# Kernel tuning notes

Measured on AMD Instinct MI355X. Metric: run time of the kernel, lower is better.

The kernel has to match this reference:

```python
import jax, jax.numpy as jnp
import numpy as np

EPS = 1e-8
CHUNK = 4096  # points per chunk, mirrors max_v_per_call-style tiling


def _winding_field(verts, faces, points):
    """Winding-number occupancy of `points` w.r.t. triangle mesh (verts, faces).
    verts: (V,3) f32, faces: (F,3) int, points: (P,3) f32 -> (P,) f32."""
    fv = verts[faces]                      # (F,3,3) face corner coords
    A = fv[:, 1] - fv[:, 0]
    B = fv[:, 2] - fv[:, 1]
    C = fv[:, 0] - fv[:, 2]

    def corner_angle(u, v):
        c = -jnp.sum(u * v, axis=1) / (EPS + jnp.linalg.norm(u, axis=1) * jnp.linalg.norm(v, axis=1))
        return jnp.arccos(jnp.clip(c, -1.0, 1.0))

    angles = jnp.stack([corner_angle(C, A), corner_angle(A, B), corner_angle(B, C)], axis=1)  # (F,3)
    s2 = jnp.sin(2.0 * angles)
    w = s2 / (jnp.sum(s2, axis=-1, keepdims=True) + EPS)
    w = (w[:, [2, 0, 1]] + w[:, [1, 2, 0]]) / 2.0     # dual area weights per corner

    fn = jnp.cross(A, B)                                # unnormalized face normals (F,3)
    areas = 0.5 * jnp.linalg.norm(fn, axis=1)           # face areas (F,)

    V = verts.shape[0]
    idx = faces.reshape(-1)                             # (3F,)
    # dual area per vertex: scatter-sum corner dual areas
    dual_v = jax.ops.segment_sum((w * areas[:, None]).reshape(-1), idx, num_segments=V)  # (V,)
    # area-weighted vertex normals: scatter-sum face normals to corners, then normalize
    vn = jax.ops.segment_sum(jnp.repeat(fn, 3, axis=0), idx, num_segments=V)             # (V,3)
    vn = vn / (jnp.linalg.norm(vn, axis=1, keepdims=True) + EPS)
    na = vn * dual_v[:, None]                           # areaic normals (V,3)

    def chunk_fn(p):                                    # p: (CHUNK,3)
        diff = verts[None, :, :] - p[:, None, :]        # (CHUNK,V,3)  == (p_vert - q_point)
        r = jnp.linalg.norm(diff, axis=-1, keepdims=True)
        E = diff / (r ** 3 + EPS)                       # 1/r^2 field direction
        return jnp.einsum('mvc,vc->m', E, na)           # (CHUNK,)

    P = points.shape[0]
    wf = jax.lax.map(chunk_fn, points.reshape(P // CHUNK, CHUNK, 3)).reshape(P)
    return wf / (4.0 * jnp.pi)


def setup_inputs() -> dict:
    key = jax.random.key(0)
    k1, k2, k3 = jax.random.split(key, 3)
    V, F, P = 8192, 16384, 32768
    verts = jax.random.uniform(k1, (V, 3), dtype=jnp.float32) * 2.0 - 1.0
    points = jax.random.uniform(k3, (P, 3), dtype=jnp.float32) * 2.0 - 1.0
    faces = jax.random.randint(k2, (F, 3), 0, V)
    return {"verts": verts, "points": points, "faces": faces}


def reference(verts, points, faces):
    return _winding_field(verts, faces, points)
```

## Files before the change

### kernel.cpp

```cpp
#include <hip/hip_runtime.h>
#include <math.h>

#define EPS32   1e-8f
#define INV4PI  0.07957747154594767f
#define TPB     256
#define VSLICE  128
#define PPT     4

__global__ void zero2_k(float* __restrict__ a, int na,
                        float* __restrict__ b, int nb) {
    int i = blockIdx.x * TPB + threadIdx.x;
    if (i < na) a[i] = 0.0f;
    else if (i < na + nb) b[i - na] = 0.0f;
}

__device__ __forceinline__ float n3_f32(float x, float y, float z) {
    return __fsqrt_rn(__fadd_rn(__fadd_rn(__fmul_rn(x, x), __fmul_rn(y, y)),
                                __fmul_rn(z, z)));
}

__global__ void face_k(const float* __restrict__ verts,
                       const int*   __restrict__ faces,
                       float*       __restrict__ acc, int F) {
    int f = blockIdx.x * TPB + threadIdx.x;
    if (f >= F) return;
    int i0 = faces[3*f+0], i1 = faces[3*f+1], i2 = faces[3*f+2];
    float p0x = verts[3*i0], p0y = verts[3*i0+1], p0z = verts[3*i0+2];
    float p1x = verts[3*i1], p1y = verts[3*i1+1], p1z = verts[3*i1+2];
    float p2x = verts[3*i2], p2y = verts[3*i2+1], p2z = verts[3*i2+2];

    float Ax = __fsub_rn(p1x, p0x), Ay = __fsub_rn(p1y, p0y), Az = __fsub_rn(p1z, p0z);
    float Bx = __fsub_rn(p2x, p1x), By = __fsub_rn(p2y, p1y), Bz = __fsub_rn(p2z, p1z);
    float Cx = __fsub_rn(p0x, p2x), Cy = __fsub_rn(p0y, p2y), Cz = __fsub_rn(p0z, p2z);

    float nA = n3_f32(Ax, Ay, Az);
    float nB = n3_f32(Bx, By, Bz);
    float nC = n3_f32(Cx, Cy, Cz);

    auto s2f = [](float ux, float uy, float uz, float vx, float vy, float vz,
                  float nu, float nv) {
        float d   = __fadd_rn(__fadd_rn(__fmul_rn(ux, vx), __fmul_rn(uy, vy)),
                              __fmul_rn(uz, vz));
        float den = __fadd_rn(EPS32, __fmul_rn(nu, nv));
        float c   = __fdiv_rn(-d, den);
        c = fminf(1.0f, fmaxf(-1.0f, c));
        float th  = (float)acos((double)c);
        return (float)sin(2.0 * (double)th);
    };
    float s0 = s2f(Cx,Cy,Cz, Ax,Ay,Az, nC, nA);
    float s1 = s2f(Ax,Ay,Az, Bx,By,Bz, nA, nB);
    float s2 = s2f(Bx,By,Bz, Cx,Cy,Cz, nB, nC);

    float ssum  = __fadd_rn(__fadd_rn(s0, s1), s2);
    float wden  = __fadd_rn(ssum, EPS32);
    float w0 = __fdiv_rn(s0, wden);
    float w1 = __fdiv_rn(s1, wden);
    float w2 = __fdiv_rn(s2, wden);

    float fnx = __fsub_rn(__fmul_rn(Ay, Bz), __fmul_rn(Az, By));
    float fny = __fsub_rn(__fmul_rn(Az, Bx), __fmul_rn(Ax, Bz));
    float fnz = __fsub_rn(__fmul_rn(Ax, By), __fmul_rn(Ay, Bx));
    float area = __fmul_rn(0.5f, n3_f32(fnx, fny, fnz));

    float c0 = __fmul_rn(__fmul_rn(__fadd_rn(w2, w1), 0.5f), area);
    float c1 = __fmul_rn(__fmul_rn(__fadd_rn(w0, w2), 0.5f), area);
    float c2 = __fmul_rn(__fmul_rn(__fadd_rn(w1, w0), 0.5f), area);

    atomicAdd(&acc[4*i0+0], c0);
    atomicAdd(&acc[4*i0+1], fnx); atomicAdd(&acc[4*i0+2], fny); atomicAdd(&acc[4*i0+3], fnz);
    atomicAdd(&acc[4*i1+0], c1);
    atomicAdd(&acc[4*i1+1], fnx); atomicAdd(&acc[4*i1+2], fny); atomicAdd(&acc[4*i1+3], fnz);
    atomicAdd(&acc[4*i2+0], c2);
    atomicAdd(&acc[4*i2+1], fnx); atomicAdd(&acc[4*i2+2], fny); atomicAdd(&acc[4*i2+3], fnz);
}

__global__ void vert_k(const float* __restrict__ verts,
                       const float* __restrict__ acc,
                       float*       __restrict__ vna, int V) {
    int v = blockIdx.x * TPB + threadIdx.x;
    if (v >= V) return;
    float dual = acc[4*v+0];
    float nx = acc[4*v+1], ny = acc[4*v+2], nz = acc[4*v+3];
    float den = __fadd_rn(n3_f32(nx, ny, nz), EPS32);
    float sx = __fmul_rn(__fdiv_rn(nx, den), dual);
    float sy = __fmul_rn(__fdiv_rn(ny, den), dual);
    float sz = __fmul_rn(__fdiv_rn(nz, den), dual);
    vna[6*v+0] = verts[3*v+0];
    vna[6*v+1] = verts[3*v+1];
    vna[6*v+2] = verts[3*v+2];
    vna[6*v+3] = __fmul_rn(sx, INV4PI);
    vna[6*v+4] = __fmul_rn(sy, INV4PI);
    vna[6*v+5] = __fmul_rn(sz, INV4PI);
}

__global__ __launch_bounds__(TPB) void wind_k(const float* __restrict__ points,
                                              const float* __restrict__ vna,
                                              float*       __restrict__ out,
                                              int P, int V) {
    const int vbase = blockIdx.y * VSLICE;
    const int nv    = min(VSLICE, V - vbase);
    const float* __restrict__ g = vna + (size_t)6*vbase;

    const int pb = blockIdx.x * (TPB*PPT) + threadIdx.x;
    float px[PPT], py[PPT], pz[PPT], accp[PPT];
    bool  ok[PPT];
#pragma unroll
    for (int k = 0; k < PPT; ++k) {
        int p = pb + k*TPB;
        ok[k] = p < P;
        px[k] = ok[k] ? points[3*p+0] : 0.f;
        py[k] = ok[k] ? points[3*p+1] : 0.f;
        pz[k] = ok[k] ? points[3*p+2] : 0.f;
        accp[k] = 0.0f;
    }

    auto interact = [](float vx, float vy, float vz,
                       float nx, float ny, float nz,
                       float qx, float qy, float qz, float& a) {
        float dx = vx - qx, dy = vy - qy, dz = vz - qz;
        float r2 = fmaf(dx, dx, fmaf(dy, dy, dz*dz));
        float r  = __builtin_amdgcn_sqrtf(r2);
        float denom = fmaf(r, r2, EPS32);
        float num   = fmaf(dx, nx, fmaf(dy, ny, dz*nz));
        a = fmaf(num, __builtin_amdgcn_rcpf(denom), a);
    };

    const int npair = nv >> 1;
#pragma unroll 4
    for (int j = 0; j < npair; ++j) {
        float v0x = g[12*j+ 0], v0y = g[12*j+ 1], v0z = g[12*j+ 2];
        float n0x = g[12*j+ 3], n0y = g[12*j+ 4], n0z = g[12*j+ 5];
        float v1x = g[12*j+ 6], v1y = g[12*j+ 7], v1z = g[12*j+ 8];
        float n1x = g[12*j+ 9], n1y = g[12*j+10], n1z = g[12*j+11];
#pragma unroll
        for (int k = 0; k < PPT; ++k)
            interact(v0x,v0y,v0z, n0x,n0y,n0z, px[k],py[k],pz[k], accp[k]);
#pragma unroll
        for (int k = 0; k < PPT; ++k)
            interact(v1x,v1y,v1z, n1x,n1y,n1z, px[k],py[k],pz[k], accp[k]);
    }
    if (nv & 1) {
        int i = nv - 1;
#pragma unroll
        for (int k = 0; k < PPT; ++k)
            interact(g[6*i],g[6*i+1],g[6*i+2], g[6*i+3],g[6*i+4],g[6*i+5],
                     px[k],py[k],pz[k], accp[k]);
    }

#pragma unroll
    for (int k = 0; k < PPT; ++k)
        if (ok[k]) atomicAdd(&out[pb + k*TPB], accp[k]);
}

extern "C" void kernel_launch(void* const* d_in, const int* in_sizes, int n_in,
                              void* d_out, int out_size, void* d_ws, size_t ws_size,
                              hipStream_t stream) {
    const float* verts  = (const float*)d_in[0];
    const float* points = (const float*)d_in[1];
    const int*   faces  = (const int*)  d_in[2];
    float*       out    = (float*)d_out;

    const int V = in_sizes[0] / 3;
    const int P = in_sizes[1] / 3;
    const int F = in_sizes[2] / 3;

    float* acc = (float*)d_ws;
    float* vna = (float*)((char*)d_ws + (size_t)4*V*sizeof(float));

    zero2_k<<<(P + 4*V + TPB-1)/TPB, TPB, 0, stream>>>(out, P, acc, 4*V);
    face_k<<<(F + TPB-1)/TPB, TPB, 0, stream>>>(verts, faces, acc, F);
    vert_k<<<(V + TPB-1)/TPB, TPB, 0, stream>>>(verts, acc, vna, V);

    dim3 grid((P + TPB*PPT - 1)/(TPB*PPT), (V + VSLICE-1)/VSLICE);
    wind_k<<<grid, TPB, 0, stream>>>(points, vna, out, P, V);
}
```

Measured before the change: 162.6 us.

## Fuse vertex normalization into winding kernel via shared memory; raise points per thread

Drops the separate per-vertex kernel and has each winding block compute its slice of normalized area-weighted normals straight into LDS, then read vertex data from shared memory instead of global loads. Points per thread rise from 4 to 8, with the inner unroll cut to 2 to contain register pressure. This removes a launch and a global round trip. In exchange, every x-block recomputes the slice normalization, and the larger per-thread tile halves the grid's x dimension and raises register use.

```diff
diff --git a/kernel.cpp b/kernel.cpp
--- a/kernel.cpp
+++ b/kernel.cpp
@@ -5,7 +5,7 @@
 #define INV4PI  0.07957747154594767f
 #define TPB     256
 #define VSLICE  128
-#define PPT     4
+#define PPT     8
 
 __global__ void zero2_k(float* __restrict__ a, int na,
                         float* __restrict__ b, int nb) {
@@ -74,32 +74,34 @@
     atomicAdd(&acc[4*i2+1], fnx); atomicAdd(&acc[4*i2+2], fny); atomicAdd(&acc[4*i2+3], fnz);
 }
 
-__global__ void vert_k(const float* __restrict__ verts,
-                       const float* __restrict__ acc,
-                       float*       __restrict__ vna, int V) {
-    int v = blockIdx.x * TPB + threadIdx.x;
-    if (v >= V) return;
-    float dual = acc[4*v+0];
-    float nx = acc[4*v+1], ny = acc[4*v+2], nz = acc[4*v+3];
-    float den = __fadd_rn(n3_f32(nx, ny, nz), EPS32);
-    float sx = __fmul_rn(__fdiv_rn(nx, den), dual);
-    float sy = __fmul_rn(__fdiv_rn(ny, den), dual);
-    float sz = __fmul_rn(__fdiv_rn(nz, den), dual);
-    vna[6*v+0] = verts[3*v+0];
-    vna[6*v+1] = verts[3*v+1];
-    vna[6*v+2] = verts[3*v+2];
-    vna[6*v+3] = __fmul_rn(sx, INV4PI);
-    vna[6*v+4] = __fmul_rn(sy, INV4PI);
-    vna[6*v+5] = __fmul_rn(sz, INV4PI);
-}
-
 __global__ __launch_bounds__(TPB) void wind_k(const float* __restrict__ points,
-                                              const float* __restrict__ vna,
+                                              const float* __restrict__ verts,
+                                              const float* __restrict__ acc,
                                               float*       __restrict__ out,
                                               int P, int V) {
+    __shared__ float sv[VSLICE*6];
     const int vbase = blockIdx.y * VSLICE;
     const int nv    = min(VSLICE, V - vbase);
-    const float* __restrict__ g = vna + (size_t)6*vbase;
+
+    {
+        int i = threadIdx.x;
+        if (i < nv) {
+            int v = vbase + i;
+            float dual = acc[4*v+0];
+            float nx = acc[4*v+1], ny = acc[4*v+2], nz = acc[4*v+3];
+            float den = __fadd_rn(n3_f32(nx, ny, nz), EPS32);
+            float sx = __fmul_rn(__fdiv_rn(nx, den), dual);
+            float sy = __fmul_rn(__fdiv_rn(ny, den), dual);
+            float sz = __fmul_rn(__fdiv_rn(nz, den), dual);
+            sv[6*i+0] = verts[3*v+0];
+            sv[6*i+1] = verts[3*v+1];
+            sv[6*i+2] = verts[3*v+2];
+            sv[6*i+3] = __fmul_rn(sx, INV4PI);
+            sv[6*i+4] = __fmul_rn(sy, INV4PI);
+            sv[6*i+5] = __fmul_rn(sz, INV4PI);
+        }
+    }
+    __syncthreads();
 
     const int pb = blockIdx.x * (TPB*PPT) + threadIdx.x;
     float px[PPT], py[PPT], pz[PPT], accp[PPT];
@@ -126,12 +128,12 @@
     };
 
     const int npair = nv >> 1;
-#pragma unroll 4
+#pragma unroll 2
     for (int j = 0; j < npair; ++j) {
-        float v0x = g[12*j+ 0], v0y = g[12*j+ 1], v0z = g[12*j+ 2];
-        float n0x = g[12*j+ 3], n0y = g[12*j+ 4], n0z = g[12*j+ 5];
-        float v1x = g[12*j+ 6], v1y = g[12*j+ 7], v1z = g[12*j+ 8];
-        float n1x = g[12*j+ 9], n1y = g[12*j+10], n1z = g[12*j+11];
+        float v0x = sv[12*j+ 0], v0y = sv[12*j+ 1], v0z = sv[12*j+ 2];
+        float n0x = sv[12*j+ 3], n0y = sv[12*j+ 4], n0z = sv[12*j+ 5];
+        float v1x = sv[12*j+ 6], v1y = sv[12*j+ 7], v1z = sv[12*j+ 8];
+        float n1x = sv[12*j+ 9], n1y = sv[12*j+10], n1z = sv[12*j+11];
 #pragma unroll
         for (int k = 0; k < PPT; ++k)
             interact(v0x,v0y,v0z, n0x,n0y,n0z, px[k],py[k],pz[k], accp[k]);
@@ -143,7 +145,7 @@
         int i = nv - 1;
 #pragma unroll
         for (int k = 0; k < PPT; ++k)
-            interact(g[6*i],g[6*i+1],g[6*i+2], g[6*i+3],g[6*i+4],g[6*i+5],
+            interact(sv[6*i],sv[6*i+1],sv[6*i+2], sv[6*i+3],sv[6*i+4],sv[6*i+5],
                      px[k],py[k],pz[k], accp[k]);
     }
 
@@ -165,12 +167,10 @@
     const int F = in_sizes[2] / 3;
 
     float* acc = (float*)d_ws;
-    float* vna = (float*)((char*)d_ws + (size_t)4*V*sizeof(float));
 
     zero2_k<<<(P + 4*V + TPB-1)/TPB, TPB, 0, stream>>>(out, P, acc, 4*V);
     face_k<<<(F + TPB-1)/TPB, TPB, 0, stream>>>(verts, faces, acc, F);
-    vert_k<<<(V + TPB-1)/TPB, TPB, 0, stream>>>(verts, acc, vna, V);
 
     dim3 grid((P + TPB*PPT - 1)/(TPB*PPT), (V + VSLICE-1)/VSLICE);
-    wind_k<<<grid, TPB, 0, stream>>>(points, vna, out, P, V);
+    wind_k<<<grid, TPB, 0, stream>>>(points, verts, acc, out, P, V);
 }
```

Measured after the change: 155.6 us. 4.3% less time.
